# Performance work log

Measured on AMD Instinct MI355X. Metric: run time of the kernel, lower is better.

The kernel has to match this reference:

```python
import math
import jax, jax.numpy as jnp
import numpy as np

NQ, NK = 4096, 8192
D_Q, D_K, D_ATTN, H, D_OUT = 256, 256, 64, 4, 256


def setup_inputs() -> dict:
    key = jax.random.key(0)
    ks = jax.random.split(key, 10)
    s = 0.02
    return {
        "x_Q": jax.random.normal(ks[0], (NQ, D_Q), jnp.float32),
        "x_K": jax.random.normal(ks[1], (NK, D_K), jnp.float32),
        "mask": jax.random.randint(ks[2], (NQ, NK), 0, 2, jnp.int32),
        # per-head projection weights, stored as (H, in, out) so y = x @ W
        "Wq": jax.random.normal(ks[3], (H, D_Q, D_ATTN), jnp.float32) * s,
        "Wk": jax.random.normal(ks[4], (H, D_K, D_ATTN), jnp.float32) * s,
        "Wv": jax.random.normal(ks[5], (H, D_K, D_ATTN), jnp.float32) * s,
        # per-head gate: Linear(d_Q, 1) + sigmoid
        "Wg": jax.random.normal(ks[6], (H, D_Q), jnp.float32) * s,
        "bg": jax.random.normal(ks[7], (H,), jnp.float32) * s,
        # output projection Linear(d_attn, d_out) with bias
        "Wo": jax.random.normal(ks[8], (D_ATTN, D_OUT), jnp.float32) * s,
        "bo": jax.random.normal(ks[9], (D_OUT,), jnp.float32) * s,
    }


def reference(x_Q, x_K, mask, Wq, Wk, Wv, Wg, bg, Wo, bo):
    m = mask.astype(x_Q.dtype)  # (NQ, NK) 0/1
    # Stacked per-head projections (original loops over heads)
    Q = jnp.einsum("nq,hqa->hna", x_Q, Wq)  # (H, NQ, A)
    K = jnp.einsum("mk,hka->hma", x_K, Wk)  # (H, NK, A)
    V = jnp.einsum("mk,hka->hma", x_K, Wv)  # (H, NK, A)
    scale = 1.0 / math.sqrt(D_ATTN)
    scores = jnp.einsum("hna,hma->hnm", Q, K) * scale  # (H, NQ, NK)
    # masked_softmax: (mask * x).masked_fill(mask == 0, -inf) then softmax over keys
    X = jnp.where(m == 0, -jnp.inf, m * scores)
    attn = jax.nn.softmax(X, axis=-1)
    heads = jnp.einsum("hnm,hma->hna", attn, V)  # (H, NQ, A)
    gates = jax.nn.sigmoid(jnp.einsum("nq,hq->hn", x_Q, Wg) + bg[:, None])  # (H, NQ)
    combined = jnp.einsum("hna,hn->na", heads, gates)  # (NQ, A)
    return combined @ Wo + bo  # (NQ, D_OUT)
```

## Files before the change

### kernel.cpp

```cpp
#include <hip/hip_runtime.h>
#include <hip/hip_bf16.h>

#define NQ 4096
#define NK 8192
#define DQK 256
#define DA 64
#define NH 4
#define DOUT 256
#define KSPLIT 16
#define KLEN (NK / KSPLIT)
#define NQT (NQ / 32)
#define LOG2E 1.44269504088896340736f
#define QSCALE (0.125f * LOG2E)

typedef __attribute__((ext_vector_type(8))) short bf16x8;
typedef __attribute__((ext_vector_type(4))) float f32x4;
typedef __attribute__((ext_vector_type(4))) _Float16 f16x4;

__device__ inline unsigned short f2bf(float f) {
  union { float f; unsigned u; } v; v.f = f;
  unsigned r = v.u + 0x7fff + ((v.u >> 16) & 1);
  return (unsigned short)(r >> 16);
}

__global__ __launch_bounds__(256) void prep_kernel(
    const int* __restrict__ mask, unsigned* __restrict__ bitsT,
    const float* __restrict__ xQ, const float* __restrict__ xK,
    const float* __restrict__ Wq, const float* __restrict__ Wk,
    const float* __restrict__ Wv,
    unsigned short* __restrict__ Qp, unsigned short* __restrict__ Kp,
    _Float16* __restrict__ Vf) {
  __shared__ __align__(16) unsigned short Wt[64][264];

  if (blockIdx.x < 8192) {
    const int NW = 8192 * 4;
    int wid = blockIdx.x * 4 + (threadIdx.x >> 6);
    int lane = threadIdx.x & 63;
    for (int j = 0; j < 2; ++j) {
      int v[8];
#pragma unroll
      for (int u = 0; u < 8; ++u) {
        int c = wid + (j * 8 + u) * NW;
        v[u] = mask[(size_t)(c >> 7) * NK + (c & 127) * 64 + lane];
      }
#pragma unroll
      for (int u = 0; u < 8; ++u) {
        unsigned long long b = __ballot(v[u] != 0);
        int c = wid + (j * 8 + u) * NW;
        int n = c >> 7, ch = c & 127;
        if (lane == 0)  bitsT[(size_t)(2 * ch) * NQ + n] = (unsigned)b;
        if (lane == 32) bitsT[(size_t)(2 * ch + 1) * NQ + n] = (unsigned)(b >> 32);
      }
    }
    return;
  }

  int b = blockIdx.x - 8192;
  int proj, h, rb;
  if (b < 64)        { proj = 0; h = b >> 4;  rb = b & 15; }
  else if (b < 192)  { proj = 1; b -= 64;  h = b >> 5; rb = b & 31; }
  else               { proj = 2; b -= 192; h = b >> 5; rb = b & 31; }
  const float* x = (proj == 0) ? xQ : xK;
  const float* W = (proj == 0 ? Wq : (proj == 1 ? Wk : Wv)) + (size_t)h * 256 * 64;

  for (int i = threadIdx.x; i < 16384; i += 256)
    Wt[i & 63][i >> 6] = f2bf(W[i]);
  __syncthreads();

  int lane = threadIdx.x & 63, wv = threadIdx.x >> 6;
  int quad = lane >> 4, n16 = lane & 15;
  int r0 = rb * 256 + wv * 64;

  f32x4 acc[4][4];
#pragma unroll
  for (int mt = 0; mt < 4; ++mt)
#pragma unroll
    for (int nt = 0; nt < 4; ++nt)
      acc[mt][nt] = (f32x4){0.f, 0.f, 0.f, 0.f};

#pragma unroll
  for (int it = 0; it < 8; ++it) {
    const int k0 = it * 32;
    bf16x8 af[4];
#pragma unroll
    for (int mt = 0; mt < 4; ++mt) {
      const float* xp = x + (size_t)(r0 + mt * 16 + n16) * 256 + k0 + quad * 8;
      const float4 a0 = *(const float4*)xp;
      const float4 a1 = *(const float4*)(xp + 4);
      bf16x8 a;
      a[0] = (short)f2bf(a0.x); a[1] = (short)f2bf(a0.y);
      a[2] = (short)f2bf(a0.z); a[3] = (short)f2bf(a0.w);
      a[4] = (short)f2bf(a1.x); a[5] = (short)f2bf(a1.y);
      a[6] = (short)f2bf(a1.z); a[7] = (short)f2bf(a1.w);
      af[mt] = a;
    }
    bf16x8 bfr[4];
#pragma unroll
    for (int nt = 0; nt < 4; ++nt)
      bfr[nt] = *(const bf16x8*)&Wt[nt * 16 + n16][k0 + quad * 8];
#pragma unroll
    for (int mt = 0; mt < 4; ++mt)
#pragma unroll
      for (int nt = 0; nt < 4; ++nt)
        acc[mt][nt] = __builtin_amdgcn_mfma_f32_16x16x32_bf16(
            af[mt], bfr[nt], acc[mt][nt], 0, 0, 0);
  }

  if (proj < 2) {
    unsigned short* outp =
        (proj == 0 ? Qp : Kp) + (size_t)h * (size_t)(proj == 0 ? NQ : NK) * 64;
    const float sc = (proj == 0) ? QSCALE : 1.0f;
#pragma unroll
    for (int mt = 0; mt < 4; ++mt)
#pragma unroll
      for (int nt = 0; nt < 4; ++nt)
#pragma unroll
        for (int r = 0; r < 4; ++r) {
          int row = r0 + mt * 16 + quad * 4 + r;
          int col = nt * 16 + n16;
          outp[(size_t)row * 64 + col] = f2bf(acc[mt][nt][r] * sc);
        }
  } else {
#pragma unroll
    for (int mt = 0; mt < 4; ++mt) {
      int tile = h * 256 + ((r0 + mt * 16) >> 5);
      int kr = mt & 1;
#pragma unroll
      for (int nt = 0; nt < 4; ++nt) {
        f16x4 pk;
        pk[0] = (_Float16)acc[mt][nt][0]; pk[1] = (_Float16)acc[mt][nt][1];
        pk[2] = (_Float16)acc[mt][nt][2]; pk[3] = (_Float16)acc[mt][nt][3];
        *(f16x4*)&Vf[(((size_t)tile * 8 + kr * 4 + nt) * 64 + lane) * 4] = pk;
      }
    }
  }
}

__global__ __launch_bounds__(256, 4) void attn_kernel(
    const unsigned short* __restrict__ Qp, const unsigned short* __restrict__ Kp,
    const _Float16* __restrict__ Vf, const unsigned* __restrict__ bitsT,
    _Float16* __restrict__ Opart, float* __restrict__ Lpart) {
  int b = blockIdx.x;
  int qg = b & 31, ks = (b >> 5) & 15, h = b >> 9;
  int wv = threadIdx.x >> 6, lane = threadIdx.x & 63;
  int quad = lane >> 4, n16 = lane & 15;
  int qt = qg * 4 + wv;
  int qb = qt * 32;

  bf16x8 qf[2][2];
#pragma unroll
  for (int qc = 0; qc < 2; ++qc)
#pragma unroll
    for (int c = 0; c < 2; ++c)
      qf[qc][c] = *(const bf16x8*)&Qp[((size_t)h * NQ + qb + qc * 16 + n16) * 64 +
                                      c * 32 + quad * 8];

  f32x4 o[4][2];
#pragma unroll
  for (int dt = 0; dt < 4; ++dt)
#pragma unroll
    for (int qc = 0; qc < 2; ++qc) o[dt][qc] = (f32x4){0.f, 0.f, 0.f, 0.f};
  float ls[2] = {0.f, 0.f};

  const unsigned short* Kptr =
      Kp + (size_t)h * NK * 64 + (size_t)(ks * KLEN + n16) * 64 + quad * 8;
  const _Float16* Vbase = Vf + ((size_t)h * 256 + ks * 16) * 2048 + lane * 4;
  const unsigned* bT = bitsT + (size_t)(ks * 16) * NQ + qb;

#pragma unroll 2
  for (int kb = 0; kb < KLEN / 32; ++kb) {
    unsigned wqa0 = bT[(size_t)kb * NQ + n16];
    unsigned wqa1 = bT[(size_t)kb * NQ + 16 + n16];

    const unsigned short* Kg = Kptr + (size_t)kb * 32 * 64;
    bf16x8 kf[2][2];
#pragma unroll
    for (int kr = 0; kr < 2; ++kr)
#pragma unroll
      for (int c = 0; c < 2; ++c)
        kf[kr][c] = *(const bf16x8*)(Kg + kr * 16 * 64 + c * 32);

    const _Float16* Vg = Vbase + (size_t)kb * 2048;
    f16x4 vf[4][2];
#pragma unroll
    for (int kr = 0; kr < 2; ++kr)
#pragma unroll
      for (int dt = 0; dt < 4; ++dt)
        vf[dt][kr] = *(const f16x4*)(Vg + (kr * 4 + dt) * 256);

    f32x4 s[2][2];
#pragma unroll
    for (int kr = 0; kr < 2; ++kr)
#pragma unroll
      for (int qc = 0; qc < 2; ++qc) {
        f32x4 acc = (f32x4){0.f, 0.f, 0.f, 0.f};
        acc = __builtin_amdgcn_mfma_f32_16x16x32_bf16(kf[kr][0], qf[qc][0], acc, 0, 0, 0);
        acc = __builtin_amdgcn_mfma_f32_16x16x32_bf16(kf[kr][1], qf[qc][1], acc, 0, 0, 0);
        s[kr][qc] = acc;
      }

#pragma unroll
    for (int qc = 0; qc < 2; ++qc) {
      unsigned wq = (qc == 0 ? wqa0 : wqa1) >> (quad * 4);
      f16x4 pf[2];
#pragma unroll
      for (int kr = 0; kr < 2; ++kr) {
        float e0 = __builtin_amdgcn_exp2f(s[kr][qc][0]);
        float e1 = __builtin_amdgcn_exp2f(s[kr][qc][1]);
        float e2 = __builtin_amdgcn_exp2f(s[kr][qc][2]);
        float e3 = __builtin_amdgcn_exp2f(s[kr][qc][3]);
        e0 = (wq & (1u << (kr * 16 + 0))) ? e0 : 0.f;
        e1 = (wq & (1u << (kr * 16 + 1))) ? e1 : 0.f;
        e2 = (wq & (1u << (kr * 16 + 2))) ? e2 : 0.f;
        e3 = (wq & (1u << (kr * 16 + 3))) ? e3 : 0.f;
        ls[qc] += (e0 + e1) + (e2 + e3);
        f16x4 p;
        p[0] = (_Float16)e0; p[1] = (_Float16)e1;
        p[2] = (_Float16)e2; p[3] = (_Float16)e3;
        pf[kr] = p;
      }
#pragma unroll
      for (int dt = 0; dt < 4; ++dt) {
        o[dt][qc] = __builtin_amdgcn_mfma_f32_16x16x16f16(vf[dt][0], pf[0],
                                                          o[dt][qc], 0, 0, 0);
        o[dt][qc] = __builtin_amdgcn_mfma_f32_16x16x16f16(vf[dt][1], pf[1],
                                                          o[dt][qc], 0, 0, 0);
      }
    }
  }

#pragma unroll
  for (int qc = 0; qc < 2; ++qc) {
    ls[qc] += __shfl_xor(ls[qc], 16);
    ls[qc] += __shfl_xor(ls[qc], 32);
  }

  const size_t tile = ((size_t)h * NQT + qt) * KSPLIT + ks;
#pragma unroll
  for (int qc = 0; qc < 2; ++qc) {
#pragma unroll
    for (int dt = 0; dt < 4; ++dt) {
      size_t idx = (tile * 32 + qc * 16 + n16) * 64 + dt * 16 + quad * 4;
      f16x4 ov;
      ov[0] = (_Float16)o[dt][qc][0]; ov[1] = (_Float16)o[dt][qc][1];
      ov[2] = (_Float16)o[dt][qc][2]; ov[3] = (_Float16)o[dt][qc][3];
      *(f16x4*)&Opart[idx] = ov;
    }
  }
  if (quad == 0) {
    Lpart[tile * 32 + n16] = ls[0];
    Lpart[tile * 32 + 16 + n16] = ls[1];
  }
}

__global__ __launch_bounds__(256) void combine_kernel(
    const _Float16* __restrict__ Opart, const float* __restrict__ Lpart,
    const float* __restrict__ xQ, const float* __restrict__ Wg,
    const float* __restrict__ bg, const float* __restrict__ Wo,
    const float* __restrict__ bo, float* __restrict__ out) {
  __shared__ float comb[16][64];
  __shared__ float gred[16][4][4];
  __shared__ float glds[16][4];
  int nb = blockIdx.x;
  int tid = threadIdx.x;

  {
    int r = tid >> 4, hh = (tid >> 2) & 3, c = tid & 3;
    const float* xp = xQ + (size_t)(nb * 16 + r) * 256 + c * 64;
    const float* wp = Wg + hh * 256 + c * 64;
    float s = 0.f;
#pragma unroll
    for (int e = 0; e < 64; ++e) s = fmaf(xp[e], wp[e], s);
    gred[r][hh][c] = s;
  }
  __syncthreads();
  if (tid < 64) {
    int r = tid >> 2, hh = tid & 3;
    float s = gred[r][hh][0] + gred[r][hh][1] + gred[r][hh][2] + gred[r][hh][3];
    glds[r][hh] = 1.f / (1.f + __expf(-(s + bg[hh])));
  }
  __syncthreads();

  int r4 = tid >> 6, a = tid & 63;
  int qt = nb >> 1, rbase = (nb & 1) * 16;

  for (int p = 0; p < 4; ++p) {
    int r = p * 4 + r4;
    int rl = rbase + r;
    float csum = 0.f;
#pragma unroll
    for (int h = 0; h < NH; ++h) {
      size_t t0 = ((size_t)h * NQT + qt) * KSPLIT;
      float accO = 0.f, lt = 0.f;
#pragma unroll
      for (int s = 0; s < KSPLIT; ++s) {
        size_t t = t0 + s;
        accO += (float)Opart[(t * 32 + rl) * 64 + a];
        lt += Lpart[t * 32 + rl];
      }
      csum += glds[r][h] * accO / lt;
    }
    comb[r][a] = csum;
  }
  __syncthreads();

  int j = tid;
  float accv[16];
#pragma unroll
  for (int r = 0; r < 16; ++r) accv[r] = bo[j];
  for (int aa = 0; aa < 64; ++aa) {
    float w = Wo[(size_t)aa * 256 + j];
#pragma unroll
    for (int r = 0; r < 16; ++r) accv[r] = fmaf(comb[r][aa], w, accv[r]);
  }
#pragma unroll
  for (int r = 0; r < 16; ++r)
    out[(size_t)(nb * 16 + r) * 256 + j] = accv[r];
}

extern "C" void kernel_launch(void* const* d_in, const int* in_sizes, int n_in,
                              void* d_out, int out_size, void* d_ws, size_t ws_size,
                              hipStream_t stream) {
  const float* xQ  = (const float*)d_in[0];
  const float* xK  = (const float*)d_in[1];
  const int*   mask= (const int*)d_in[2];
  const float* Wq  = (const float*)d_in[3];
  const float* Wk  = (const float*)d_in[4];
  const float* Wv  = (const float*)d_in[5];
  const float* Wg  = (const float*)d_in[6];
  const float* bg  = (const float*)d_in[7];
  const float* Wo  = (const float*)d_in[8];
  const float* bo  = (const float*)d_in[9];
  float* out = (float*)d_out;

  char* ws = (char*)d_ws;
  unsigned short* Qp   = (unsigned short*)(ws + 0);
  unsigned short* Kp   = (unsigned short*)(ws + 2097152);
  _Float16*       Vfp  = (_Float16*)(ws + 6291456);
  unsigned*       bitsT= (unsigned*)(ws + 10485760);
  float*          Lp   = (float*)(ws + 14680064);
  _Float16*       Op   = (_Float16*)(ws + 15728640);

  prep_kernel<<<dim3(8512), dim3(256), 0, stream>>>(
      mask, bitsT, xQ, xK, Wq, Wk, Wv, Qp, Kp, Vfp);
  attn_kernel<<<dim3(2048), dim3(256), 0, stream>>>(Qp, Kp, Vfp, bitsT, Op, Lp);
  combine_kernel<<<dim3(NQ / 16), dim3(256), 0, stream>>>(Op, Lp, xQ, Wg, bg,
                                                          Wo, bo, out);
}
```

Before: 418.4 us.

## Fuse prep, attention and combine into one persistent cooperative kernel with grid syncs

Replaces the three kernel launches with a single cooperative persistent kernel. Work units are looped over the grid and phases are separated by grid.sync. The projection GEMM now reads weights straight from global memory with per-element bf16 conversion instead of staging them in LDS. The combine phase is re-tiled to 4 rows per unit. This removes launch gaps and the tails between kernels, at the cost of grid-wide barriers, strided uncoalesced weight loads, and a fixed grid sized for occupancy.

```diff
diff --git a/kernel.cpp b/kernel.cpp
--- a/kernel.cpp
+++ b/kernel.cpp
@@ -1,17 +1,15 @@
 #include <hip/hip_runtime.h>
-#include <hip/hip_bf16.h>
+#include <hip/hip_cooperative_groups.h>
+
+namespace cg = cooperative_groups;
 
 #define NQ 4096
 #define NK 8192
-#define DQK 256
-#define DA 64
 #define NH 4
-#define DOUT 256
 #define KSPLIT 16
 #define KLEN (NK / KSPLIT)
 #define NQT (NQ / 32)
-#define LOG2E 1.44269504088896340736f
-#define QSCALE (0.125f * LOG2E)
+#define QSCALE (0.125f * 1.44269504088896340736f)
 
 typedef __attribute__((ext_vector_type(8))) short bf16x8;
 typedef __attribute__((ext_vector_type(4))) float f32x4;
@@ -23,299 +21,283 @@
   return (unsigned short)(r >> 16);
 }
 
-__global__ __launch_bounds__(256) void prep_kernel(
+__global__ __launch_bounds__(256, 4) void mega_kernel(
     const int* __restrict__ mask, unsigned* __restrict__ bitsT,
     const float* __restrict__ xQ, const float* __restrict__ xK,
     const float* __restrict__ Wq, const float* __restrict__ Wk,
-    const float* __restrict__ Wv,
-    unsigned short* __restrict__ Qp, unsigned short* __restrict__ Kp,
-    _Float16* __restrict__ Vf) {
-  __shared__ __align__(16) unsigned short Wt[64][264];
-
-  if (blockIdx.x < 8192) {
-    const int NW = 8192 * 4;
-    int wid = blockIdx.x * 4 + (threadIdx.x >> 6);
-    int lane = threadIdx.x & 63;
-    for (int j = 0; j < 2; ++j) {
+    const float* __restrict__ Wv, const float* __restrict__ Wg,
+    const float* __restrict__ bg, const float* __restrict__ Wo,
+    const float* __restrict__ bo, unsigned short* __restrict__ Qp,
+    unsigned short* __restrict__ Kp, _Float16* __restrict__ Vf,
+    _Float16* __restrict__ Opart, float* __restrict__ Lpart,
+    float* __restrict__ out) {
+  cg::grid_group grid = cg::this_grid();
+  const int G = gridDim.x;
+  const int tid = threadIdx.x;
+  const int wv = tid >> 6, lane = tid & 63;
+  const int quad = lane >> 4, n16 = lane & 15;
+
+  __shared__ float comb[4][64];
+  __shared__ float glds[4][4];
+
+  for (int u = blockIdx.x; u < 640; u += G) {
+    int b = u, proj, h, rb;
+    if (b < 128)      { proj = 0; h = b >> 5; rb = b & 31; }
+    else if (b < 384) { proj = 1; b -= 128; h = b >> 6; rb = b & 63; }
+    else              { proj = 2; b -= 384; h = b >> 6; rb = b & 63; }
+    const float* x = (proj == 0) ? xQ : xK;
+    const float* W = (proj == 0 ? Wq : (proj == 1 ? Wk : Wv)) + (size_t)h * 16384;
+    const int r0 = rb * 128 + wv * 32;
+
+    f32x4 acc[2][4];
+#pragma unroll
+    for (int mt = 0; mt < 2; ++mt)
+#pragma unroll
+      for (int nt = 0; nt < 4; ++nt) acc[mt][nt] = (f32x4){0.f, 0.f, 0.f, 0.f};
+
+#pragma unroll
+    for (int it = 0; it < 8; ++it) {
+      const int k0 = it * 32;
+      bf16x8 af[2];
+#pragma unroll
+      for (int mt = 0; mt < 2; ++mt) {
+        const float* xp = x + (size_t)(r0 + mt * 16 + n16) * 256 + k0 + quad * 8;
+        const float4 a0 = *(const float4*)xp;
+        const float4 a1 = *(const float4*)(xp + 4);
+        bf16x8 a;
+        a[0] = (short)f2bf(a0.x); a[1] = (short)f2bf(a0.y);
+        a[2] = (short)f2bf(a0.z); a[3] = (short)f2bf(a0.w);
+        a[4] = (short)f2bf(a1.x); a[5] = (short)f2bf(a1.y);
+        a[6] = (short)f2bf(a1.z); a[7] = (short)f2bf(a1.w);
+        af[mt] = a;
+      }
+      bf16x8 bfr[4];
+#pragma unroll
+      for (int nt = 0; nt < 4; ++nt) {
+        bf16x8 bb;
+#pragma unroll
+        for (int i = 0; i < 8; ++i)
+          bb[i] = (short)f2bf(W[(size_t)(k0 + quad * 8 + i) * 64 + nt * 16 + n16]);
+        bfr[nt] = bb;
+      }
+#pragma unroll
+      for (int mt = 0; mt < 2; ++mt)
+#pragma unroll
+        for (int nt = 0; nt < 4; ++nt)
+          acc[mt][nt] = __builtin_amdgcn_mfma_f32_16x16x32_bf16(
+              af[mt], bfr[nt], acc[mt][nt], 0, 0, 0);
+    }
+
+    if (proj < 2) {
+      unsigned short* outp =
+          (proj == 0 ? Qp : Kp) + (size_t)h * (size_t)(proj == 0 ? NQ : NK) * 64;
+      const float sc = (proj == 0) ? QSCALE : 1.0f;
+#pragma unroll
+      for (int mt = 0; mt < 2; ++mt)
+#pragma unroll
+        for (int nt = 0; nt < 4; ++nt)
+#pragma unroll
+          for (int r = 0; r < 4; ++r) {
+            int row = r0 + mt * 16 + quad * 4 + r;
+            int col = nt * 16 + n16;
+            outp[(size_t)row * 64 + col] = f2bf(acc[mt][nt][r] * sc);
+          }
+    } else {
+#pragma unroll
+      for (int mt = 0; mt < 2; ++mt) {
+        int tile = h * 256 + ((r0 + mt * 16) >> 5);
+        int kr = ((r0 + mt * 16) >> 4) & 1;
+#pragma unroll
+        for (int nt = 0; nt < 4; ++nt) {
+          f16x4 pk;
+          pk[0] = (_Float16)acc[mt][nt][0]; pk[1] = (_Float16)acc[mt][nt][1];
+          pk[2] = (_Float16)acc[mt][nt][2]; pk[3] = (_Float16)acc[mt][nt][3];
+          *(f16x4*)&Vf[(((size_t)tile * 8 + kr * 4 + nt) * 64 + lane) * 4] = pk;
+        }
+      }
+    }
+  }
+
+  {
+    const int NWv = G * 4;
+    const int wid = blockIdx.x * 4 + wv;
+    for (int g8 = wid; g8 < 65536; g8 += NWv) {
       int v[8];
 #pragma unroll
+      for (int u = 0; u < 8; ++u)
+        v[u] = mask[(size_t)(g8 * 8 + u) * 64 + lane];
+#pragma unroll
       for (int u = 0; u < 8; ++u) {
-        int c = wid + (j * 8 + u) * NW;
-        v[u] = mask[(size_t)(c >> 7) * NK + (c & 127) * 64 + lane];
-      }
-#pragma unroll
-      for (int u = 0; u < 8; ++u) {
-        unsigned long long b = __ballot(v[u] != 0);
-        int c = wid + (j * 8 + u) * NW;
-        int n = c >> 7, ch = c & 127;
-        if (lane == 0)  bitsT[(size_t)(2 * ch) * NQ + n] = (unsigned)b;
-        if (lane == 32) bitsT[(size_t)(2 * ch + 1) * NQ + n] = (unsigned)(b >> 32);
-      }
-    }
-    return;
+        unsigned long long bl = __ballot(v[u] != 0);
+        int c = g8 * 8 + u, n = c >> 7, ch = c & 127;
+        if (lane == 0)  bitsT[(size_t)(2 * ch) * NQ + n] = (unsigned)bl;
+        if (lane == 32) bitsT[(size_t)(2 * ch + 1) * NQ + n] = (unsigned)(bl >> 32);
+      }
+    }
   }
 
-  int b = blockIdx.x - 8192;
-  int proj, h, rb;
-  if (b < 64)        { proj = 0; h = b >> 4;  rb = b & 15; }
-  else if (b < 192)  { proj = 1; b -= 64;  h = b >> 5; rb = b & 31; }
-  else               { proj = 2; b -= 192; h = b >> 5; rb = b & 31; }
-  const float* x = (proj == 0) ? xQ : xK;
-  const float* W = (proj == 0 ? Wq : (proj == 1 ? Wk : Wv)) + (size_t)h * 256 * 64;
-
-  for (int i = threadIdx.x; i < 16384; i += 256)
-    Wt[i & 63][i >> 6] = f2bf(W[i]);
-  __syncthreads();
-
-  int lane = threadIdx.x & 63, wv = threadIdx.x >> 6;
-  int quad = lane >> 4, n16 = lane & 15;
-  int r0 = rb * 256 + wv * 64;
-
-  f32x4 acc[4][4];
-#pragma unroll
-  for (int mt = 0; mt < 4; ++mt)
-#pragma unroll
-    for (int nt = 0; nt < 4; ++nt)
-      acc[mt][nt] = (f32x4){0.f, 0.f, 0.f, 0.f};
-
-#pragma unroll
-  for (int it = 0; it < 8; ++it) {
-    const int k0 = it * 32;
-    bf16x8 af[4];
-#pragma unroll
-    for (int mt = 0; mt < 4; ++mt) {
-      const float* xp = x + (size_t)(r0 + mt * 16 + n16) * 256 + k0 + quad * 8;
-      const float4 a0 = *(const float4*)xp;
-      const float4 a1 = *(const float4*)(xp + 4);
-      bf16x8 a;
-      a[0] = (short)f2bf(a0.x); a[1] = (short)f2bf(a0.y);
-      a[2] = (short)f2bf(a0.z); a[3] = (short)f2bf(a0.w);
-      a[4] = (short)f2bf(a1.x); a[5] = (short)f2bf(a1.y);
-      a[6] = (short)f2bf(a1.z); a[7] = (short)f2bf(a1.w);
-      af[mt] = a;
-    }
-    bf16x8 bfr[4];
-#pragma unroll
-    for (int nt = 0; nt < 4; ++nt)
-      bfr[nt] = *(const bf16x8*)&Wt[nt * 16 + n16][k0 + quad * 8];
-#pragma unroll
-    for (int mt = 0; mt < 4; ++mt)
-#pragma unroll
-      for (int nt = 0; nt < 4; ++nt)
-        acc[mt][nt] = __builtin_amdgcn_mfma_f32_16x16x32_bf16(
-            af[mt], bfr[nt], acc[mt][nt], 0, 0, 0);
+  __threadfence();
+  grid.sync();
+  __threadfence();
+
+  for (int u = blockIdx.x; u < 2048; u += G) {
+    const int qg = u & 31, ks = (u >> 5) & 15, h = u >> 9;
+    const int qt = qg * 4 + wv, qb = qt * 32;
+
+    bf16x8 qf[2][2];
+#pragma unroll
+    for (int qc = 0; qc < 2; ++qc)
+#pragma unroll
+      for (int c = 0; c < 2; ++c)
+        qf[qc][c] = *(const bf16x8*)&Qp[((size_t)h * NQ + qb + qc * 16 + n16) * 64 +
+                                        c * 32 + quad * 8];
+
+    f32x4 o[4][2];
+#pragma unroll
+    for (int dt = 0; dt < 4; ++dt)
+#pragma unroll
+      for (int qc = 0; qc < 2; ++qc) o[dt][qc] = (f32x4){0.f, 0.f, 0.f, 0.f};
+    float ls[2] = {0.f, 0.f};
+
+    const unsigned short* Kptr =
+        Kp + (size_t)h * NK * 64 + (size_t)(ks * KLEN + n16) * 64 + quad * 8;
+    const _Float16* Vbase = Vf + ((size_t)h * 256 + ks * 16) * 2048 + lane * 4;
+    const unsigned* bT = bitsT + (size_t)(ks * 16) * NQ + qb;
+
+#pragma unroll 2
+    for (int kb = 0; kb < KLEN / 32; ++kb) {
+      unsigned wqa0 = bT[(size_t)kb * NQ + n16];
+      unsigned wqa1 = bT[(size_t)kb * NQ + 16 + n16];
+
+      const unsigned short* Kg = Kptr + (size_t)kb * 32 * 64;
+      bf16x8 kf[2][2];
+#pragma unroll
+      for (int kr = 0; kr < 2; ++kr)
+#pragma unroll
+        for (int c = 0; c < 2; ++c)
+          kf[kr][c] = *(const bf16x8*)(Kg + kr * 16 * 64 + c * 32);
+
+      const _Float16* Vg = Vbase + (size_t)kb * 2048;
+      f16x4 vf[4][2];
+#pragma unroll
+      for (int kr = 0; kr < 2; ++kr)
+#pragma unroll
+        for (int dt = 0; dt < 4; ++dt)
+          vf[dt][kr] = *(const f16x4*)(Vg + (kr * 4 + dt) * 256);
+
+      f32x4 s[2][2];
+#pragma unroll
+      for (int kr = 0; kr < 2; ++kr)
+#pragma unroll
+        for (int qc = 0; qc < 2; ++qc) {
+          f32x4 a2 = (f32x4){0.f, 0.f, 0.f, 0.f};
+          a2 = __builtin_amdgcn_mfma_f32_16x16x32_bf16(kf[kr][0], qf[qc][0], a2, 0, 0, 0);
+          a2 = __builtin_amdgcn_mfma_f32_16x16x32_bf16(kf[kr][1], qf[qc][1], a2, 0, 0, 0);
+          s[kr][qc] = a2;
+        }
+
+#pragma unroll
+      for (int qc = 0; qc < 2; ++qc) {
+        unsigned wq = (qc == 0 ? wqa0 : wqa1) >> (quad * 4);
+        f16x4 pf[2];
+#pragma unroll
+        for (int kr = 0; kr < 2; ++kr) {
+          float e0 = __builtin_amdgcn_exp2f(s[kr][qc][0]);
+          float e1 = __builtin_amdgcn_exp2f(s[kr][qc][1]);
+          float e2 = __builtin_amdgcn_exp2f(s[kr][qc][2]);
+          float e3 = __builtin_amdgcn_exp2f(s[kr][qc][3]);
+          e0 = (wq & (1u << (kr * 16 + 0))) ? e0 : 0.f;
+          e1 = (wq & (1u << (kr * 16 + 1))) ? e1 : 0.f;
+          e2 = (wq & (1u << (kr * 16 + 2))) ? e2 : 0.f;
+          e3 = (wq & (1u << (kr * 16 + 3))) ? e3 : 0.f;
+          ls[qc] += (e0 + e1) + (e2 + e3);
+          f16x4 p;
+          p[0] = (_Float16)e0; p[1] = (_Float16)e1;
+          p[2] = (_Float16)e2; p[3] = (_Float16)e3;
+          pf[kr] = p;
+        }
+#pragma unroll
+        for (int dt = 0; dt < 4; ++dt) {
+          o[dt][qc] = __builtin_amdgcn_mfma_f32_16x16x16f16(vf[dt][0], pf[0],
+                                                            o[dt][qc], 0, 0, 0);
+          o[dt][qc] = __builtin_amdgcn_mfma_f32_16x16x16f16(vf[dt][1], pf[1],
+                                                            o[dt][qc], 0, 0, 0);
+        }
+      }
+    }
+
+#pragma unroll
+    for (int qc = 0; qc < 2; ++qc) {
+      ls[qc] += __shfl_xor(ls[qc], 16);
+      ls[qc] += __shfl_xor(ls[qc], 32);
+    }
+
+    const size_t tile = ((size_t)h * NQT + qt) * KSPLIT + ks;
+#pragma unroll
+    for (int qc = 0; qc < 2; ++qc) {
+#pragma unroll
+      for (int dt = 0; dt < 4; ++dt) {
+        size_t idx = (tile * 32 + qc * 16 + n16) * 64 + dt * 16 + quad * 4;
+        f16x4 ov;
+        ov[0] = (_Float16)o[dt][qc][0]; ov[1] = (_Float16)o[dt][qc][1];
+        ov[2] = (_Float16)o[dt][qc][2]; ov[3] = (_Float16)o[dt][qc][3];
+        *(f16x4*)&Opart[idx] = ov;
+      }
+    }
+    if (quad == 0) {
+      Lpart[tile * 32 + n16] = ls[0];
+      Lpart[tile * 32 + 16 + n16] = ls[1];
+    }
   }
 
-  if (proj < 2) {
-    unsigned short* outp =
-        (proj == 0 ? Qp : Kp) + (size_t)h * (size_t)(proj == 0 ? NQ : NK) * 64;
-    const float sc = (proj == 0) ? QSCALE : 1.0f;
-#pragma unroll
-    for (int mt = 0; mt < 4; ++mt)
-#pragma unroll
-      for (int nt = 0; nt < 4; ++nt)
-#pragma unroll
-        for (int r = 0; r < 4; ++r) {
-          int row = r0 + mt * 16 + quad * 4 + r;
-          int col = nt * 16 + n16;
-          outp[(size_t)row * 64 + col] = f2bf(acc[mt][nt][r] * sc);
-        }
-  } else {
-#pragma unroll
-    for (int mt = 0; mt < 4; ++mt) {
-      int tile = h * 256 + ((r0 + mt * 16) >> 5);
-      int kr = mt & 1;
-#pragma unroll
-      for (int nt = 0; nt < 4; ++nt) {
-        f16x4 pk;
-        pk[0] = (_Float16)acc[mt][nt][0]; pk[1] = (_Float16)acc[mt][nt][1];
-        pk[2] = (_Float16)acc[mt][nt][2]; pk[3] = (_Float16)acc[mt][nt][3];
-        *(f16x4*)&Vf[(((size_t)tile * 8 + kr * 4 + nt) * 64 + lane) * 4] = pk;
-      }
-    }
+  __threadfence();
+  grid.sync();
+  __threadfence();
+
+  for (int u = blockIdx.x; u < 1024; u += G) {
+    const int n0 = u * 4;
+    {
+      int hh = lane >> 4, seg = lane & 15;
+      const float* xp = xQ + (size_t)(n0 + wv) * 256 + seg * 16;
+      const float* wp = Wg + hh * 256 + seg * 16;
+      float gp = 0.f;
+#pragma unroll
+      for (int e = 0; e < 16; ++e) gp = fmaf(xp[e], wp[e], gp);
+      gp += __shfl_xor(gp, 1); gp += __shfl_xor(gp, 2);
+      gp += __shfl_xor(gp, 4); gp += __shfl_xor(gp, 8);
+      if (seg == 0) glds[wv][hh] = 1.f / (1.f + __expf(-(gp + bg[hh])));
+    }
+    {
+      const int n = n0 + wv, qt = n >> 5, rl = n & 31;
+      float csum = 0.f;
+#pragma unroll
+      for (int h = 0; h < NH; ++h) {
+        size_t t0 = ((size_t)h * NQT + qt) * KSPLIT;
+        float accO = 0.f, lt = 0.f;
+#pragma unroll
+        for (int s = 0; s < KSPLIT; ++s) {
+          size_t t = t0 + s;
+          accO += (float)Opart[(t * 32 + rl) * 64 + lane];
+          lt += Lpart[t * 32 + rl];
+        }
+        csum += glds[wv][h] * accO / lt;
+      }
+      comb[wv][lane] = csum;
+    }
+    __syncthreads();
+    float accv[4];
+#pragma unroll
+    for (int r = 0; r < 4; ++r) accv[r] = bo[tid];
+    for (int aa = 0; aa < 64; ++aa) {
+      float w = Wo[(size_t)aa * 256 + tid];
+#pragma unroll
+      for (int r = 0; r < 4; ++r) accv[r] = fmaf(comb[r][aa], w, accv[r]);
+    }
+#pragma unroll
+    for (int r = 0; r < 4; ++r)
+      out[(size_t)(n0 + r) * 256 + tid] = accv[r];
+    __syncthreads();
   }
-}
-
-__global__ __launch_bounds__(256, 4) void attn_kernel(
-    const unsigned short* __restrict__ Qp, const unsigned short* __restrict__ Kp,
-    const _Float16* __restrict__ Vf, const unsigned* __restrict__ bitsT,
-    _Float16* __restrict__ Opart, float* __restrict__ Lpart) {
-  int b = blockIdx.x;
-  int qg = b & 31, ks = (b >> 5) & 15, h = b >> 9;
-  int wv = threadIdx.x >> 6, lane = threadIdx.x & 63;
-  int quad = lane >> 4, n16 = lane & 15;
-  int qt = qg * 4 + wv;
-  int qb = qt * 32;
-
-  bf16x8 qf[2][2];
-#pragma unroll
-  for (int qc = 0; qc < 2; ++qc)
-#pragma unroll
-    for (int c = 0; c < 2; ++c)
-      qf[qc][c] = *(const bf16x8*)&Qp[((size_t)h * NQ + qb + qc * 16 + n16) * 64 +
-                                      c * 32 + quad * 8];
-
-  f32x4 o[4][2];
-#pragma unroll
-  for (int dt = 0; dt < 4; ++dt)
-#pragma unroll
-    for (int qc = 0; qc < 2; ++qc) o[dt][qc] = (f32x4){0.f, 0.f, 0.f, 0.f};
-  float ls[2] = {0.f, 0.f};
-
-  const unsigned short* Kptr =
-      Kp + (size_t)h * NK * 64 + (size_t)(ks * KLEN + n16) * 64 + quad * 8;
-  const _Float16* Vbase = Vf + ((size_t)h * 256 + ks * 16) * 2048 + lane * 4;
-  const unsigned* bT = bitsT + (size_t)(ks * 16) * NQ + qb;
-
-#pragma unroll 2
-  for (int kb = 0; kb < KLEN / 32; ++kb) {
-    unsigned wqa0 = bT[(size_t)kb * NQ + n16];
-    unsigned wqa1 = bT[(size_t)kb * NQ + 16 + n16];
-
-    const unsigned short* Kg = Kptr + (size_t)kb * 32 * 64;
-    bf16x8 kf[2][2];
-#pragma unroll
-    for (int kr = 0; kr < 2; ++kr)
-#pragma unroll
-      for (int c = 0; c < 2; ++c)
-        kf[kr][c] = *(const bf16x8*)(Kg + kr * 16 * 64 + c * 32);
-
-    const _Float16* Vg = Vbase + (size_t)kb * 2048;
-    f16x4 vf[4][2];
-#pragma unroll
-    for (int kr = 0; kr < 2; ++kr)
-#pragma unroll
-      for (int dt = 0; dt < 4; ++dt)
-        vf[dt][kr] = *(const f16x4*)(Vg + (kr * 4 + dt) * 256);
-
-    f32x4 s[2][2];
-#pragma unroll
-    for (int kr = 0; kr < 2; ++kr)
-#pragma unroll
-      for (int qc = 0; qc < 2; ++qc) {
-        f32x4 acc = (f32x4){0.f, 0.f, 0.f, 0.f};
-        acc = __builtin_amdgcn_mfma_f32_16x16x32_bf16(kf[kr][0], qf[qc][0], acc, 0, 0, 0);
-        acc = __builtin_amdgcn_mfma_f32_16x16x32_bf16(kf[kr][1], qf[qc][1], acc, 0, 0, 0);
-        s[kr][qc] = acc;
-      }
-
-#pragma unroll
-    for (int qc = 0; qc < 2; ++qc) {
-      unsigned wq = (qc == 0 ? wqa0 : wqa1) >> (quad * 4);
-      f16x4 pf[2];
-#pragma unroll
-      for (int kr = 0; kr < 2; ++kr) {
-        float e0 = __builtin_amdgcn_exp2f(s[kr][qc][0]);
-        float e1 = __builtin_amdgcn_exp2f(s[kr][qc][1]);
-        float e2 = __builtin_amdgcn_exp2f(s[kr][qc][2]);
-        float e3 = __builtin_amdgcn_exp2f(s[kr][qc][3]);
-        e0 = (wq & (1u << (kr * 16 + 0))) ? e0 : 0.f;
-        e1 = (wq & (1u << (kr * 16 + 1))) ? e1 : 0.f;
-        e2 = (wq & (1u << (kr * 16 + 2))) ? e2 : 0.f;
-        e3 = (wq & (1u << (kr * 16 + 3))) ? e3 : 0.f;
-        ls[qc] += (e0 + e1) + (e2 + e3);
-        f16x4 p;
-        p[0] = (_Float16)e0; p[1] = (_Float16)e1;
-        p[2] = (_Float16)e2; p[3] = (_Float16)e3;
-        pf[kr] = p;
-      }
-#pragma unroll
-      for (int dt = 0; dt < 4; ++dt) {
-        o[dt][qc] = __builtin_amdgcn_mfma_f32_16x16x16f16(vf[dt][0], pf[0],
-                                                          o[dt][qc], 0, 0, 0);
-        o[dt][qc] = __builtin_amdgcn_mfma_f32_16x16x16f16(vf[dt][1], pf[1],
-                                                          o[dt][qc], 0, 0, 0);
-      }
-    }
-  }
-
-#pragma unroll
-  for (int qc = 0; qc < 2; ++qc) {
-    ls[qc] += __shfl_xor(ls[qc], 16);
-    ls[qc] += __shfl_xor(ls[qc], 32);
-  }
-
-  const size_t tile = ((size_t)h * NQT + qt) * KSPLIT + ks;
-#pragma unroll
-  for (int qc = 0; qc < 2; ++qc) {
-#pragma unroll
-    for (int dt = 0; dt < 4; ++dt) {
-      size_t idx = (tile * 32 + qc * 16 + n16) * 64 + dt * 16 + quad * 4;
-      f16x4 ov;
-      ov[0] = (_Float16)o[dt][qc][0]; ov[1] = (_Float16)o[dt][qc][1];
-      ov[2] = (_Float16)o[dt][qc][2]; ov[3] = (_Float16)o[dt][qc][3];
-      *(f16x4*)&Opart[idx] = ov;
-    }
-  }
-  if (quad == 0) {
-    Lpart[tile * 32 + n16] = ls[0];
-    Lpart[tile * 32 + 16 + n16] = ls[1];
-  }
-}
-
-__global__ __launch_bounds__(256) void combine_kernel(
-    const _Float16* __restrict__ Opart, const float* __restrict__ Lpart,
-    const float* __restrict__ xQ, const float* __restrict__ Wg,
-    const float* __restrict__ bg, const float* __restrict__ Wo,
-    const float* __restrict__ bo, float* __restrict__ out) {
-  __shared__ float comb[16][64];
-  __shared__ float gred[16][4][4];
-  __shared__ float glds[16][4];
-  int nb = blockIdx.x;
-  int tid = threadIdx.x;
-
-  {
-    int r = tid >> 4, hh = (tid >> 2) & 3, c = tid & 3;
-    const float* xp = xQ + (size_t)(nb * 16 + r) * 256 + c * 64;
-    const float* wp = Wg + hh * 256 + c * 64;
-    float s = 0.f;
-#pragma unroll
-    for (int e = 0; e < 64; ++e) s = fmaf(xp[e], wp[e], s);
-    gred[r][hh][c] = s;
-  }
-  __syncthreads();
-  if (tid < 64) {
-    int r = tid >> 2, hh = tid & 3;
-    float s = gred[r][hh][0] + gred[r][hh][1] + gred[r][hh][2] + gred[r][hh][3];
-    glds[r][hh] = 1.f / (1.f + __expf(-(s + bg[hh])));
-  }
-  __syncthreads();
-
-  int r4 = tid >> 6, a = tid & 63;
-  int qt = nb >> 1, rbase = (nb & 1) * 16;
-
-  for (int p = 0; p < 4; ++p) {
-    int r = p * 4 + r4;
-    int rl = rbase + r;
-    float csum = 0.f;
-#pragma unroll
-    for (int h = 0; h < NH; ++h) {
-      size_t t0 = ((size_t)h * NQT + qt) * KSPLIT;
-      float accO = 0.f, lt = 0.f;
-#pragma unroll
-      for (int s = 0; s < KSPLIT; ++s) {
-        size_t t = t0 + s;
-        accO += (float)Opart[(t * 32 + rl) * 64 + a];
-        lt += Lpart[t * 32 + rl];
-      }
-      csum += glds[r][h] * accO / lt;
-    }
-    comb[r][a] = csum;
-  }
-  __syncthreads();
-
-  int j = tid;
-  float accv[16];
-#pragma unroll
-  for (int r = 0; r < 16; ++r) accv[r] = bo[j];
-  for (int aa = 0; aa < 64; ++aa) {
-    float w = Wo[(size_t)aa * 256 + j];
-#pragma unroll
-    for (int r = 0; r < 16; ++r) accv[r] = fmaf(comb[r][aa], w, accv[r]);
-  }
-#pragma unroll
-  for (int r = 0; r < 16; ++r)
-    out[(size_t)(nb * 16 + r) * 256 + j] = accv[r];
 }
 
 extern "C" void kernel_launch(void* const* d_in, const int* in_sizes, int n_in,
@@ -336,14 +318,22 @@
   char* ws = (char*)d_ws;
   unsigned short* Qp   = (unsigned short*)(ws + 0);
   unsigned short* Kp   = (unsigned short*)(ws + 2097152);
-  _Float16*       Vfp  = (_Float16*)(ws + 6291456);
+  _Float16*       Vf   = (_Float16*)(ws + 6291456);
   unsigned*       bitsT= (unsigned*)(ws + 10485760);
   float*          Lp   = (float*)(ws + 14680064);
   _Float16*       Op   = (_Float16*)(ws + 15728640);
 
-  prep_kernel<<<dim3(8512), dim3(256), 0, stream>>>(
-      mask, bitsT, xQ, xK, Wq, Wk, Wv, Qp, Kp, Vfp);
-  attn_kernel<<<dim3(2048), dim3(256), 0, stream>>>(Qp, Kp, Vfp, bitsT, Op, Lp);
-  combine_kernel<<<dim3(NQ / 16), dim3(256), 0, stream>>>(Op, Lp, xQ, Wg, bg,
-                                                          Wo, bo, out);
+  int maxB = 0;
+  hipOccupancyMaxActiveBlocksPerMultiprocessor(
+      &maxB, reinterpret_cast<const void*>(mega_kernel), 256, 0);
+  if (maxB < 1) maxB = 1;
+  int gridB = maxB * 256;
+
+  void* args[] = {
+      (void*)&mask, (void*)&bitsT, (void*)&xQ, (void*)&xK,
+      (void*)&Wq, (void*)&Wk, (void*)&Wv, (void*)&Wg, (void*)&bg,
+      (void*)&Wo, (void*)&bo, (void*)&Qp, (void*)&Kp, (void*)&Vf,
+      (void*)&Op, (void*)&Lp, (void*)&out};
+  hipLaunchCooperativeKernel(reinterpret_cast<void*>(mega_kernel),
+                             dim3(gridB), dim3(256), args, 0, stream);
 }
```

Measured after the change: 892.8 us. 2.13x slower.
